# Kernel optimization log

Hardware: AMD Instinct MI355X
Metric: run time of the kernel (lower is better)

The kernel has to match this reference:

```python
import jax, jax.numpy as jnp
import numpy as np

N, K, C, D4, HID, HEAD, DEPTH = 40000, 16, 128, 32, 512, 256, 4
EPS = 1e-5  # BatchNorm eps; eval mode with running_mean=0, running_var=1


def _bn(x, g, b):
    # eval-mode BatchNorm1d with fresh running stats (mean=0, var=1)
    return x * (g / np.sqrt(1.0 + EPS)) + b


def _mlp(x, w1, b1, w2, g, b):
    # Linear -> GELU -> Linear(no bias) -> BN
    return _bn(jax.nn.gelu(x @ w1 + b1) @ w2, g, b)


def _lfp(x, lxyz, knn, proj, coor, scale, g, b):
    # LFP: Linear(no bias) -> la_spse_a4 (neighbor gather + anisotropic spatial
    # positional encoding, one PE channel per 4 feature channels, max-pool over k) -> BN
    xp = x @ proj                                   # (N, C)
    xn = xp[knn]                                    # (N, K, C) irregular gather
    rel3 = (lxyz[knn] - lxyz[:, None])[..., :3]     # (N, K, 3)
    pe = jnp.einsum('nkc,cd->nkd', rel3, coor) * jnp.square(scale)  # (N, K, D4)
    out = jnp.max(xn.reshape(N, K, D4, 4) + pe[..., None], axis=1).reshape(N, C)
    return _bn(out, g, b)


def _knn_spse4(lxyz, feat, knn, m_sp, c, h):
    # knn_spse_4: squared anisotropic spatial distances (3 learned 4-d directions
    # per output channel, 12 params) + per-channel color (3) + height (1) weighted
    # squared diffs, averaged over k neighbors; caller takes sqrt.
    rel4 = lxyz[knn] - lxyz[:, None]                # (N, K, 4)
    relf = feat[knn] - feat[:, None]                # (N, K, 4) = color(3)+height(1)
    dirs = m_sp.reshape(3, 4, C)
    e = jnp.zeros((N, K, C), jnp.float32)
    for j in range(3):  # fixed small loop over 3 learned directions
        e = e + jnp.square(jnp.einsum('nkc,cd->nkd', rel4, dirs[j]))
    e = e + jnp.einsum('nki,id->nkd', jnp.square(relf[..., :3]), jnp.square(c))
    e = e + jnp.square(relf[..., 3:4]) * jnp.square(h)
    return jnp.sqrt(e.mean(axis=1))                 # (N, C)


def setup_inputs():
    key = jax.random.key(0)
    ks = jax.random.split(key, 32)
    rn = lambda i, s, sc=0.02: jax.random.normal(ks[i], s, jnp.float32) * sc
    gm = lambda i, s: 1.0 + jax.random.normal(ks[i], s, jnp.float32) * 0.1
    return {
        'x': rn(0, (N, 4), 1.0),
        'xyz': jax.random.uniform(ks[1], (N, 3), jnp.float32),
        'knn': jax.random.randint(ks[2], (N, K), 0, N, jnp.int32),
        'spse_m': rn(3, (12, C), 0.5),
        'spse_c': rn(4, (3, C), 0.5),
        'spse_h': rn(5, (C,), 0.5),
        'nbr_bn0_g': gm(6, (C,)), 'nbr_bn0_b': rn(7, (C,)),
        'nbr_w1': rn(8, (C, 2 * C)), 'nbr_b1': rn(9, (2 * C,)),
        'nbr_w2': rn(10, (2 * C, C)),
        'nbr_bn_g': gm(11, (C,)), 'nbr_bn_b': rn(12, (C,)),
        'lfp_proj': rn(13, (DEPTH, C, C)),
        'lfp_coor': rn(14, (DEPTH, 3, D4), 0.5),
        'lfp_scale': 0.1 + rn(15, (DEPTH, D4), 0.01),
        'lfp_bng': gm(16, (DEPTH, C)), 'lfp_bnb': rn(17, (DEPTH, C)),
        'mlp_w1': rn(18, (3, C, HID)), 'mlp_b1': rn(19, (3, HID)),
        'mlp_w2': rn(20, (3, HID, C)),
        'mlp_bng': gm(21, (3, C)), 'mlp_bnb': rn(22, (3, C)),
        'post_bn_g': gm(23, (C,)), 'post_bn_b': rn(24, (C,)),
        'post_w': rn(25, (C, HEAD)),
    }


def reference(x, xyz, knn, spse_m, spse_c, spse_h, nbr_bn0_g, nbr_bn0_b,
              nbr_w1, nbr_b1, nbr_w2, nbr_bn_g, nbr_bn_b,
              lfp_proj, lfp_coor, lfp_scale, lfp_bng, lfp_bnb,
              mlp_w1, mlp_b1, mlp_w2, mlp_bng, mlp_bnb,
              post_bn_g, post_bn_b, post_w):
    # Stage.forward, first==last stage, eval mode (no drop_path, no closs).
    lxyz = jnp.pad(xyz, ((0, 0), (0, 1)))  # cor_std = 1.0
    nbr = _knn_spse4(lxyz, x, knn, spse_m, spse_c, spse_h)
    nbr = _bn(nbr, nbr_bn0_g, nbr_bn0_b)
    nbr = jax.nn.gelu(nbr @ nbr_w1 + nbr_b1) @ nbr_w2   # nbr_proj
    h = _bn(nbr, nbr_bn_g, nbr_bn_b)                    # nbr_bn; x = nbr (first stage)
    # Block: residual MLP, then DEPTH LFPs with an MLP after every 2nd LFP
    h = h + _mlp(h, mlp_w1[0], mlp_b1[0], mlp_w2[0], mlp_bng[0], mlp_bnb[0])
    for i in range(DEPTH):
        h = h + _lfp(h, lxyz, knn, lfp_proj[i], lfp_coor[i], lfp_scale[i],
                     lfp_bng[i], lfp_bnb[i])
        if i % 2 == 1:
            j = i // 2 + 1
            h = h + _mlp(h, mlp_w1[j], mlp_b1[j], mlp_w2[j], mlp_bng[j], mlp_bnb[j])
    return _bn(h, post_bn_g, post_bn_b) @ post_w        # postproj -> (N, HEAD)
```

## Files before the change

kernel.cpp:

```cpp
#include <hip/hip_runtime.h>
#include <hip/hip_bf16.h>
#include <math.h>

#define NPTS 40000
#define KNB 16
#define CH 128

typedef unsigned short u16;
typedef __attribute__((ext_vector_type(8))) short bf16x8;
typedef __attribute__((ext_vector_type(4))) float f32x4;

__device__ __forceinline__ float gelu_f(float v) {
  const float u = 0.7978845608028654f * (v + 0.044715f * v * v * v);
  const float t = __builtin_amdgcn_exp2f(-2.8853900817779268f * u);
  return v * __builtin_amdgcn_rcpf(1.0f + t);
}

__device__ __forceinline__ float bnscale(float g) {
  return g * rsqrtf(1.0f + 1e-5f);
}

__device__ __forceinline__ u16 f2bf(float x) {
  union { __hip_bfloat16 b; u16 u; } cv;
  cv.b = __float2bfloat16(x);
  return cv.u;
}

__device__ __forceinline__ float bf2f(u16 u) {
  union { float f; unsigned int i; } cv;
  cv.i = ((unsigned int)u) << 16;
  return cv.f;
}

__device__ __forceinline__ void bf16split(float x, u16& hi, u16& lo) {
  hi = f2bf(x);
  lo = f2bf(x - bf2f(hi));
}

__device__ __forceinline__ void gl2lds(const u16* gp, u16* lp) {
  __builtin_amdgcn_global_load_lds(
      (const __attribute__((address_space(1))) void*)gp,
      (__attribute__((address_space(3))) void*)lp, 16, 0, 0);
}

__global__ __launch_bounds__(128) void spse_kernel(
    const float* __restrict__ x, const float* __restrict__ xyz,
    const int* __restrict__ knn, const float* __restrict__ sm,
    const float* __restrict__ sc, const float* __restrict__ sh,
    const float* __restrict__ g0, const float* __restrict__ b0,
    u16* __restrict__ oh, u16* __restrict__ ol) {
  const int n = blockIdx.x;
  const int c = threadIdx.x;
  __shared__ float sr[KNB][3];
  __shared__ float sf[KNB][4];
  if (c < KNB) {
    const int j = knn[n * KNB + c];
    sr[c][0] = xyz[j * 3 + 0] - xyz[n * 3 + 0];
    sr[c][1] = xyz[j * 3 + 1] - xyz[n * 3 + 1];
    sr[c][2] = xyz[j * 3 + 2] - xyz[n * 3 + 2];
    float f0 = x[j * 4 + 0] - x[n * 4 + 0];
    float f1 = x[j * 4 + 1] - x[n * 4 + 1];
    float f2 = x[j * 4 + 2] - x[n * 4 + 2];
    float f3 = x[j * 4 + 3] - x[n * 4 + 3];
    sf[c][0] = f0 * f0; sf[c][1] = f1 * f1;
    sf[c][2] = f2 * f2; sf[c][3] = f3 * f3;
  }
  __syncthreads();
  const float m0 = sm[c], m1 = sm[CH + c], m2 = sm[2 * CH + c];
  const float m4 = sm[4 * CH + c], m5 = sm[5 * CH + c], m6 = sm[6 * CH + c];
  const float m8 = sm[8 * CH + c], m9 = sm[9 * CH + c], m10 = sm[10 * CH + c];
  float c0 = sc[c];          c0 *= c0;
  float c1 = sc[CH + c];     c1 *= c1;
  float c2 = sc[2 * CH + c]; c2 *= c2;
  float h2 = sh[c];          h2 *= h2;
  float e = 0.0f;
#pragma unroll
  for (int k = 0; k < KNB; k++) {
    const float r0 = sr[k][0], r1 = sr[k][1], r2 = sr[k][2];
    const float d0 = fmaf(r2, m2, fmaf(r1, m1, r0 * m0));
    const float d1 = fmaf(r2, m6, fmaf(r1, m5, r0 * m4));
    const float d2 = fmaf(r2, m10, fmaf(r1, m9, r0 * m8));
    e = fmaf(d0, d0, e);
    e = fmaf(d1, d1, e);
    e = fmaf(d2, d2, e);
    e = fmaf(sf[k][0], c0, e);
    e = fmaf(sf[k][1], c1, e);
    e = fmaf(sf[k][2], c2, e);
    e = fmaf(sf[k][3], h2, e);
  }
  const float v = sqrtf(e * (1.0f / KNB)) * bnscale(g0[c]) + b0[c];
  u16 hi, lo; bf16split(v, hi, lo);
  const size_t idx = (size_t)n * CH + c;
  oh[idx] = hi; ol[idx] = lo;
}

__global__ __launch_bounds__(256) void lfp_kernel(
    const u16* __restrict__ xp, const int* __restrict__ knn,
    const float* __restrict__ xyz, const float* __restrict__ coor,
    const float* __restrict__ scale, const float* __restrict__ g,
    const float* __restrict__ b, u16* __restrict__ hh, u16* __restrict__ hl) {
  const int t = threadIdx.x;
  const int bid = blockIdx.x;
  __shared__ int si[8][KNB];
  __shared__ float sr[8][KNB][3];
  if (t < 128) {
    const int pp = t >> 4, kk = t & 15;
    const int n = bid * 8 + pp;
    const int j = knn[n * KNB + kk];
    si[pp][kk] = j;
    sr[pp][kk][0] = xyz[j * 3 + 0] - xyz[n * 3 + 0];
    sr[pp][kk][1] = xyz[j * 3 + 1] - xyz[n * 3 + 1];
    sr[pp][kk][2] = xyz[j * 3 + 2] - xyz[n * 3 + 2];
  }
  __syncthreads();
  const int p = t >> 5, d = t & 31;
  const int n = bid * 8 + p;
  const float c0 = coor[d], c1 = coor[32 + d], c2 = coor[64 + d];
  float s2 = scale[d]; s2 *= s2;
  float a0 = -3.0e38f, a1 = -3.0e38f, a2 = -3.0e38f, a3 = -3.0e38f;
#pragma unroll
  for (int k = 0; k < KNB; k++) {
    const int j = si[p][k];
    const float pe = fmaf(sr[p][k][2], c2, fmaf(sr[p][k][1], c1, sr[p][k][0] * c0)) * s2;
    const uint2 v = *(const uint2*)(xp + (size_t)j * CH + d * 4);
    a0 = fmaxf(a0, bf2f((u16)(v.x & 0xffff)) + pe);
    a1 = fmaxf(a1, bf2f((u16)(v.x >> 16)) + pe);
    a2 = fmaxf(a2, bf2f((u16)(v.y & 0xffff)) + pe);
    a3 = fmaxf(a3, bf2f((u16)(v.y >> 16)) + pe);
  }
  const size_t off = (size_t)n * CH + d * 4;
  const float4 gg = *(const float4*)(g + d * 4);
  const float4 bb = *(const float4*)(b + d * 4);
  union { u16 a[4]; uint2 v; } oh, olo, ih, il;
  ih.v = *(const uint2*)(hh + off);
  il.v = *(const uint2*)(hl + off);
  float nv[4];
  nv[0] = bf2f(ih.a[0]) + bf2f(il.a[0]) + a0 * bnscale(gg.x) + bb.x;
  nv[1] = bf2f(ih.a[1]) + bf2f(il.a[1]) + a1 * bnscale(gg.y) + bb.y;
  nv[2] = bf2f(ih.a[2]) + bf2f(il.a[2]) + a2 * bnscale(gg.z) + bb.z;
  nv[3] = bf2f(ih.a[3]) + bf2f(il.a[3]) + a3 * bnscale(gg.w) + bb.w;
#pragma unroll
  for (int q = 0; q < 4; q++) {
    u16 hi, lo; bf16split(nv[q], hi, lo);
    oh.a[q] = hi; olo.a[q] = lo;
  }
  *(uint2*)(hh + off) = oh.v;
  *(uint2*)(hl + off) = olo.v;
}

__global__ __launch_bounds__(256) void prep_weights(
    const float* __restrict__ nw1, const float* __restrict__ nw2,
    const float* __restrict__ mw1, const float* __restrict__ mw2,
    const float* __restrict__ lproj, const float* __restrict__ pw,
    const float* __restrict__ pg, u16* __restrict__ th, u16* __restrict__ tl) {
  const int idx = blockIdx.x * 256 + threadIdx.x;
  const float* src;
  int local, Kd, Nd, dst, swz;
  float scale = 1.0f;
  if (idx < 32768)        { src = nw1; local = idx;          Kd = 128; Nd = 256; dst = 0; swz = 0; }
  else if (idx < 65536)   { src = nw2; local = idx - 32768;  Kd = 256; Nd = 128; dst = 32768; swz = 1; }
  else if (idx < 262144)  { int j = (idx - 65536) >> 16;  local = (idx - 65536) & 65535;
                            src = mw1 + j * 65536; Kd = 128; Nd = 512; dst = 65536 + j * 65536; swz = 0; }
  else if (idx < 458752)  { int j = (idx - 262144) >> 16; local = (idx - 262144) & 65535;
                            src = mw2 + j * 65536; Kd = 512; Nd = 128; dst = 262144 + j * 65536; swz = 1; }
  else if (idx < 524288)  { int i = (idx - 458752) >> 14; local = (idx - 458752) & 16383;
                            src = lproj + i * 16384; Kd = 128; Nd = 128; dst = 458752 + i * 16384; swz = 0; }
  else if (idx < 557056)  { local = idx - 524288; src = pw; Kd = 128; Nd = 256; dst = 524288; swz = 0;
                            scale = bnscale(pg[local >> 8]); }
  else return;
  const int k = local / Nd, n = local % Nd;
  const float v = src[local] * scale;
  u16 hi, lo; bf16split(v, hi, lo);
  const int ks = swz ? ((k & ~63) | ((k & 63) ^ ((n & 7) << 3))) : k;
  const int o = dst + n * Kd + ks;
  th[o] = hi; tl[o] = lo;
}

__global__ __launch_bounds__(256) void fold_pb(const float* __restrict__ pw,
                                               const float* __restrict__ pb,
                                               float* __restrict__ fb) {
  const int t = threadIdx.x;
  float a = 0.0f;
  for (int k = 0; k < 128; k++) a = fmaf(pb[k], pw[k * 256 + t], a);
  fb[t] = a;
}

template <int EPI>
__global__ __launch_bounds__(256, 2) void k128_reg(
    const u16* __restrict__ Ahi, const u16* __restrict__ Alo,
    const u16* __restrict__ Wth, const u16* __restrict__ Wtl,
    const float* __restrict__ p0, u16* __restrict__ outu,
    float* __restrict__ outf, int ostride, int ntiles) {
  const int t = threadIdx.x, lane = t & 63, w = t >> 6;
  const int col0 = blockIdx.x * 128;
  const int wm0 = (w >> 1) * 32, wn0 = (w & 1) * 64;
  const int lc = lane & 15, lq = lane >> 4;
  const int lq8 = lq * 8, lq4 = lq * 4;

  bf16x8 wh[4][4], wl[4][4];
  float bv[4];
#pragma unroll
  for (int nf = 0; nf < 4; nf++) {
    const int nr = col0 + wn0 + nf * 16 + lc;
    const u16* wr = Wth + (size_t)nr * 128;
    const u16* wr2 = Wtl + (size_t)nr * 128;
#pragma unroll
    for (int ks = 0; ks < 4; ks++) {
      wh[nf][ks] = *(const bf16x8*)(wr + ks * 32 + lq8);
      wl[nf][ks] = *(const bf16x8*)(wr2 + ks * 32 + lq8);
    }
    bv[nf] = (EPI == 0) ? 0.0f : p0[nr];
  }

  const f32x4 zz = {0.0f, 0.0f, 0.0f, 0.0f};
  for (int tile = blockIdx.y; tile < ntiles; tile += gridDim.y) {
    const int row0 = tile * 64;
    f32x4 acc[2][4];
#pragma unroll
    for (int mf = 0; mf < 2; mf++)
#pragma unroll
      for (int nf = 0; nf < 4; nf++) acc[mf][nf] = zz;
#pragma unroll
    for (int ks = 0; ks < 4; ks++) {
      bf16x8 ah[2], al[2];
#pragma unroll
      for (int mf = 0; mf < 2; mf++) {
        const size_t ao = (size_t)(row0 + wm0 + mf * 16 + lc) * 128 + ks * 32 + lq8;
        ah[mf] = *(const bf16x8*)(Ahi + ao);
        al[mf] = *(const bf16x8*)(Alo + ao);
      }
#pragma unroll
      for (int mf = 0; mf < 2; mf++)
#pragma unroll
        for (int nf = 0; nf < 4; nf++) {
          acc[mf][nf] = __builtin_amdgcn_mfma_f32_16x16x32_bf16(ah[mf], wh[nf][ks], acc[mf][nf], 0, 0, 0);
          acc[mf][nf] = __builtin_amdgcn_mfma_f32_16x16x32_bf16(ah[mf], wl[nf][ks], acc[mf][nf], 0, 0, 0);
          acc[mf][nf] = __builtin_amdgcn_mfma_f32_16x16x32_bf16(al[mf], wh[nf][ks], acc[mf][nf], 0, 0, 0);
        }
    }
#pragma unroll
    for (int mf = 0; mf < 2; mf++)
#pragma unroll
      for (int q = 0; q < 4; q++) {
        const int r = row0 + wm0 + mf * 16 + lq4 + q;
#pragma unroll
        for (int nf = 0; nf < 4; nf++) {
          const int col = col0 + wn0 + nf * 16 + lc;
          const size_t off = (size_t)r * ostride + col;
          const float v = acc[mf][nf][q];
          if (EPI == 0)      outu[off] = f2bf(v);
          else if (EPI == 1) outu[off] = f2bf(gelu_f(v + bv[nf]));
          else               outf[off] = v + bv[nf];
        }
      }
  }
}

template <int K, bool RES>
__global__ __launch_bounds__(512, 4) void gemm_w2(
    const u16* __restrict__ A, const u16* __restrict__ Wth,
    const u16* __restrict__ Wtl, const float* __restrict__ g,
    const float* __restrict__ bb, u16* __restrict__ hh, u16* __restrict__ hl) {
  __shared__ __align__(16) u16 Ws[64 * K];
  const int t = threadIdx.x, lane = t & 63, w = t >> 6;
  const int ch = blockIdx.x;
  const int row0 = blockIdx.y * 256;
  const int msub = w >> 1, cg = w & 1;
  const int lc = lane & 15, lq = lane >> 4;
  const int lq8 = lq * 8, lq4 = lq * 4;

  {
    const u16* src = Wth + (size_t)ch * 64 * K;
#pragma unroll
    for (int i = 0; i < 64 * K / 8; i += 512) {
      const int wc0 = i + w * 64;
      const int c = wc0 + lane;
      gl2lds(src + (size_t)c * 8, Ws + wc0 * 8);
    }
  }
  __syncthreads();

  const int wrow0 = msub * 64;
  const f32x4 zz = {0.0f, 0.0f, 0.0f, 0.0f};
  f32x4 acc[4][2];
#pragma unroll
  for (int mf = 0; mf < 4; mf++)
#pragma unroll
    for (int nf = 0; nf < 2; nf++) acc[mf][nf] = zz;

#pragma unroll 2
  for (int ks = 0; ks < K / 32; ks++) {
    const int e = ks * 32 + lq8;
    bf16x8 af[4];
#pragma unroll
    for (int mf = 0; mf < 4; mf++) {
      int rr = row0 + wrow0 + mf * 16 + lc;
      rr = rr < NPTS ? rr : NPTS - 1;
      af[mf] = *(const bf16x8*)(A + (size_t)rr * K + e);
    }
    bf16x8 whf[2], wlf[2];
#pragma unroll
    for (int nf = 0; nf < 2; nf++) {
      const int nr = cg * 32 + nf * 16 + lc;
      const int eo = (e & ~63) | ((e & 63) ^ ((nr & 7) << 3));
      whf[nf] = *(const bf16x8*)(Ws + nr * K + eo);
      wlf[nf] = *(const bf16x8*)(Wtl + (size_t)(ch * 64 + nr) * K + eo);
    }
#pragma unroll
    for (int mf = 0; mf < 4; mf++)
#pragma unroll
      for (int nf = 0; nf < 2; nf++) {
        acc[mf][nf] = __builtin_amdgcn_mfma_f32_16x16x32_bf16(af[mf], whf[nf], acc[mf][nf], 0, 0, 0);
        acc[mf][nf] = __builtin_amdgcn_mfma_f32_16x16x32_bf16(af[mf], wlf[nf], acc[mf][nf], 0, 0, 0);
      }
  }

  float S0[2], S1[2];
#pragma unroll
  for (int nf = 0; nf < 2; nf++) {
    const int col = ch * 64 + cg * 32 + nf * 16 + lc;
    S0[nf] = bnscale(g[col]);
    S1[nf] = bb[col];
  }
#pragma unroll
  for (int mf = 0; mf < 4; mf++)
#pragma unroll
    for (int q = 0; q < 4; q++) {
      const int r = row0 + wrow0 + mf * 16 + lq4 + q;
      if (r >= NPTS) continue;
#pragma unroll
      for (int nf = 0; nf < 2; nf++) {
        const int col = ch * 64 + cg * 32 + nf * 16 + lc;
        const size_t off = (size_t)r * CH + col;
        float v = acc[mf][nf][q] * S0[nf] + S1[nf];
        if (RES) v += bf2f(hh[off]) + bf2f(hl[off]);
        u16 hi, lo; bf16split(v, hi, lo);
        hh[off] = hi; hl[off] = lo;
      }
    }
}

extern "C" void kernel_launch(void* const* d_in, const int* in_sizes, int n_in,
                              void* d_out, int out_size, void* d_ws, size_t ws_size,
                              hipStream_t stream) {
  const float* x    = (const float*)d_in[0];
  const float* xyz  = (const float*)d_in[1];
  const int*   knn  = (const int*)d_in[2];
  const float* sm   = (const float*)d_in[3];
  const float* scc  = (const float*)d_in[4];
  const float* shh  = (const float*)d_in[5];
  const float* bn0g = (const float*)d_in[6];
  const float* bn0b = (const float*)d_in[7];
  const float* nw1  = (const float*)d_in[8];
  const float* nb1  = (const float*)d_in[9];
  const float* nw2  = (const float*)d_in[10];
  const float* nbng = (const float*)d_in[11];
  const float* nbnb = (const float*)d_in[12];
  const float* lproj  = (const float*)d_in[13];
  const float* lcoor  = (const float*)d_in[14];
  const float* lscale = (const float*)d_in[15];
  const float* lbng   = (const float*)d_in[16];
  const float* lbnb   = (const float*)d_in[17];
  const float* mw1  = (const float*)d_in[18];
  const float* mb1  = (const float*)d_in[19];
  const float* mw2  = (const float*)d_in[20];
  const float* mbng = (const float*)d_in[21];
  const float* mbnb = (const float*)d_in[22];
  const float* pg   = (const float*)d_in[23];
  const float* pb   = (const float*)d_in[24];
  const float* pw   = (const float*)d_in[25];
  float* out = (float*)d_out;

  char* ws = (char*)d_ws;
  u16*   h_hi = (u16*)(ws + 0);
  u16*   h_lo = (u16*)(ws + 10240000);
  u16*   act  = (u16*)(ws + 20480000);
  u16*   xp   = (u16*)(ws + 20480000);
  u16*   Wh   = (u16*)(ws + 61440000);
  u16*   Wl   = (u16*)(ws + 62554112);
  float* fb   = (float*)(ws + 63668224);

  const u16* nw1t   = Wh + 0;
  const u16* nw2t   = Wh + 32768;
  const u16* mw1t   = Wh + 65536;
  const u16* mw2t   = Wh + 262144;
  const u16* lprojt = Wh + 458752;
  const u16* postt  = Wh + 524288;
  const u16* nw1tl   = Wl + 0;
  const u16* nw2tl   = Wl + 32768;
  const u16* mw1tl   = Wl + 65536;
  const u16* mw2tl   = Wl + 262144;
  const u16* lprojtl = Wl + 458752;
  const u16* posttl  = Wl + 524288;

  prep_weights<<<2176, 256, 0, stream>>>(nw1, nw2, mw1, mw2, lproj, pw, pg, Wh, Wl);
  fold_pb<<<1, 256, 0, stream>>>(pw, pb, fb);

  spse_kernel<<<NPTS, 128, 0, stream>>>(x, xyz, knn, sm, scc, shh, bn0g, bn0b, h_hi, h_lo);

  k128_reg<1><<<dim3(2, 256), 256, 0, stream>>>(h_hi, h_lo, nw1t, nw1tl, nb1,
                                                act, nullptr, 256, 625);
  gemm_w2<256, false><<<dim3(2, 157), 512, 0, stream>>>(act, nw2t, nw2tl, nbng, nbnb,
                                                        h_hi, h_lo);
  k128_reg<1><<<dim3(4, 128), 256, 0, stream>>>(h_hi, h_lo, mw1t, mw1tl, mb1,
                                                act, nullptr, 512, 625);
  gemm_w2<512, true><<<dim3(2, 157), 512, 0, stream>>>(act, mw2t, mw2tl, mbng, mbnb,
                                                       h_hi, h_lo);

  for (int i = 0; i < 4; i++) {
    k128_reg<0><<<dim3(1, 512), 256, 0, stream>>>(h_hi, h_lo, lprojt + i * 16384,
                                                  lprojtl + i * 16384, nullptr,
                                                  xp, nullptr, 128, 625);
    lfp_kernel<<<5000, 256, 0, stream>>>(xp, knn, xyz, lcoor + i * 96, lscale + i * 32,
                                         lbng + i * 128, lbnb + i * 128, h_hi, h_lo);
    if (i & 1) {
      const int j = i / 2 + 1;
      k128_reg<1><<<dim3(4, 128), 256, 0, stream>>>(h_hi, h_lo, mw1t + j * 65536,
                                                    mw1tl + j * 65536, mb1 + j * 512,
                                                    act, nullptr, 512, 625);
      gemm_w2<512, true><<<dim3(2, 157), 512, 0, stream>>>(act, mw2t + j * 65536,
                                                           mw2tl + j * 65536,
                                                           mbng + j * 128, mbnb + j * 128,
                                                           h_hi, h_lo);
    }
  }

  k128_reg<2><<<dim3(2, 256), 256, 0, stream>>>(h_hi, h_lo, postt, posttl, fb,
                                                nullptr, out, 256, 625);
}
```

Measured before the change: 529.2 us.

## Restructure W2 GEMM with double-buffered K slabs, widen LFP gather, swap grid axes

The second-layer GEMM now gives each block a 64-row tile across all 128 output columns. It streams 64-wide K slabs of the high weight half into double-buffered LDS while prefetching the next A fragments, instead of staging the whole 64xK weight slice once per column chunk. The LFP kernel handles 16 points per block with 16-byte gathers of 8 channels per thread, which uses every thread in the index staging phase and widens the memory accesses. k128_reg swaps grid axes so consecutive blocks walk row tiles and the launches are remapped to match. The gains sought are better load/compute overlap, wider memory transactions and better cache locality, at the cost of more barriers and higher register use per thread.

```diff
diff --git a/kernel.cpp b/kernel.cpp
--- a/kernel.cpp
+++ b/kernel.cpp
@@ -101,11 +101,11 @@
     const float* __restrict__ b, u16* __restrict__ hh, u16* __restrict__ hl) {
   const int t = threadIdx.x;
   const int bid = blockIdx.x;
-  __shared__ int si[8][KNB];
-  __shared__ float sr[8][KNB][3];
-  if (t < 128) {
+  __shared__ int si[16][KNB];
+  __shared__ float sr[16][KNB][3];
+  {
     const int pp = t >> 4, kk = t & 15;
-    const int n = bid * 8 + pp;
+    const int n = bid * 16 + pp;
     const int j = knn[n * KNB + kk];
     si[pp][kk] = j;
     sr[pp][kk][0] = xyz[j * 3 + 0] - xyz[n * 3 + 0];
@@ -113,39 +113,40 @@
     sr[pp][kk][2] = xyz[j * 3 + 2] - xyz[n * 3 + 2];
   }
   __syncthreads();
-  const int p = t >> 5, d = t & 31;
-  const int n = bid * 8 + p;
-  const float c0 = coor[d], c1 = coor[32 + d], c2 = coor[64 + d];
-  float s2 = scale[d]; s2 *= s2;
-  float a0 = -3.0e38f, a1 = -3.0e38f, a2 = -3.0e38f, a3 = -3.0e38f;
+  const int p = t >> 4, d8 = t & 15;
+  const int n = bid * 16 + p;
+  const float c0a = coor[d8 * 2],     c1a = coor[32 + d8 * 2],     c2a = coor[64 + d8 * 2];
+  const float c0b = coor[d8 * 2 + 1], c1b = coor[32 + d8 * 2 + 1], c2b = coor[64 + d8 * 2 + 1];
+  float s2a = scale[d8 * 2];     s2a *= s2a;
+  float s2b = scale[d8 * 2 + 1]; s2b *= s2b;
+  float a[8];
+#pragma unroll
+  for (int e = 0; e < 8; e++) a[e] = -3.0e38f;
 #pragma unroll
   for (int k = 0; k < KNB; k++) {
     const int j = si[p][k];
-    const float pe = fmaf(sr[p][k][2], c2, fmaf(sr[p][k][1], c1, sr[p][k][0] * c0)) * s2;
-    const uint2 v = *(const uint2*)(xp + (size_t)j * CH + d * 4);
-    a0 = fmaxf(a0, bf2f((u16)(v.x & 0xffff)) + pe);
-    a1 = fmaxf(a1, bf2f((u16)(v.x >> 16)) + pe);
-    a2 = fmaxf(a2, bf2f((u16)(v.y & 0xffff)) + pe);
-    a3 = fmaxf(a3, bf2f((u16)(v.y >> 16)) + pe);
-  }
-  const size_t off = (size_t)n * CH + d * 4;
-  const float4 gg = *(const float4*)(g + d * 4);
-  const float4 bb = *(const float4*)(b + d * 4);
-  union { u16 a[4]; uint2 v; } oh, olo, ih, il;
-  ih.v = *(const uint2*)(hh + off);
-  il.v = *(const uint2*)(hl + off);
-  float nv[4];
-  nv[0] = bf2f(ih.a[0]) + bf2f(il.a[0]) + a0 * bnscale(gg.x) + bb.x;
-  nv[1] = bf2f(ih.a[1]) + bf2f(il.a[1]) + a1 * bnscale(gg.y) + bb.y;
-  nv[2] = bf2f(ih.a[2]) + bf2f(il.a[2]) + a2 * bnscale(gg.z) + bb.z;
-  nv[3] = bf2f(ih.a[3]) + bf2f(il.a[3]) + a3 * bnscale(gg.w) + bb.w;
-#pragma unroll
-  for (int q = 0; q < 4; q++) {
-    u16 hi, lo; bf16split(nv[q], hi, lo);
-    oh.a[q] = hi; olo.a[q] = lo;
-  }
-  *(uint2*)(hh + off) = oh.v;
-  *(uint2*)(hl + off) = olo.v;
+    const float r0 = sr[p][k][0], r1 = sr[p][k][1], r2 = sr[p][k][2];
+    const float pea = fmaf(r2, c2a, fmaf(r1, c1a, r0 * c0a)) * s2a;
+    const float peb = fmaf(r2, c2b, fmaf(r1, c1b, r0 * c0b)) * s2b;
+    const bf16x8 v = *(const bf16x8*)(xp + (size_t)j * CH + d8 * 8);
+#pragma unroll
+    for (int e = 0; e < 4; e++) a[e] = fmaxf(a[e], bf2f((u16)v[e]) + pea);
+#pragma unroll
+    for (int e = 4; e < 8; e++) a[e] = fmaxf(a[e], bf2f((u16)v[e]) + peb);
+  }
+  const size_t off = (size_t)n * CH + d8 * 8;
+  union { u16 a[8]; uint4 v; } ih, il, oh, ol;
+  ih.v = *(const uint4*)(hh + off);
+  il.v = *(const uint4*)(hl + off);
+#pragma unroll
+  for (int e = 0; e < 8; e++) {
+    const int c = d8 * 8 + e;
+    const float nv = bf2f(ih.a[e]) + bf2f(il.a[e]) + a[e] * bnscale(g[c]) + b[c];
+    u16 hi, lo; bf16split(nv, hi, lo);
+    oh.a[e] = hi; ol.a[e] = lo;
+  }
+  *(uint4*)(hh + off) = oh.v;
+  *(uint4*)(hl + off) = ol.v;
 }
 
 __global__ __launch_bounds__(256) void prep_weights(
@@ -192,7 +193,7 @@
     const float* __restrict__ p0, u16* __restrict__ outu,
     float* __restrict__ outf, int ostride, int ntiles) {
   const int t = threadIdx.x, lane = t & 63, w = t >> 6;
-  const int col0 = blockIdx.x * 128;
+  const int col0 = blockIdx.y * 128;
   const int wm0 = (w >> 1) * 32, wn0 = (w & 1) * 64;
   const int lc = lane & 15, lq = lane >> 4;
   const int lq8 = lq * 8, lq4 = lq * 4;
@@ -213,7 +214,7 @@
   }
 
   const f32x4 zz = {0.0f, 0.0f, 0.0f, 0.0f};
-  for (int tile = blockIdx.y; tile < ntiles; tile += gridDim.y) {
+  for (int tile = blockIdx.x; tile < ntiles; tile += gridDim.x) {
     const int row0 = tile * 64;
     f32x4 acc[2][4];
 #pragma unroll
@@ -257,80 +258,94 @@
 }
 
 template <int K, bool RES>
-__global__ __launch_bounds__(512, 4) void gemm_w2(
+__global__ __launch_bounds__(256, 3) void gemm_w2(
     const u16* __restrict__ A, const u16* __restrict__ Wth,
     const u16* __restrict__ Wtl, const float* __restrict__ g,
     const float* __restrict__ bb, u16* __restrict__ hh, u16* __restrict__ hl) {
-  __shared__ __align__(16) u16 Ws[64 * K];
+  __shared__ __align__(16) u16 Ws[2][128 * 64];
   const int t = threadIdx.x, lane = t & 63, w = t >> 6;
-  const int ch = blockIdx.x;
-  const int row0 = blockIdx.y * 256;
-  const int msub = w >> 1, cg = w & 1;
+  const int row0 = blockIdx.x * 64;
+  const int wm0 = (w >> 1) * 32, wn0 = (w & 1) * 64;
   const int lc = lane & 15, lq = lane >> 4;
   const int lq8 = lq * 8, lq4 = lq * 4;
 
-  {
-    const u16* src = Wth + (size_t)ch * 64 * K;
-#pragma unroll
-    for (int i = 0; i < 64 * K / 8; i += 512) {
+  const f32x4 zz = {0.0f, 0.0f, 0.0f, 0.0f};
+  f32x4 acc[2][4];
+#pragma unroll
+  for (int mf = 0; mf < 2; mf++)
+#pragma unroll
+    for (int nf = 0; nf < 4; nf++) acc[mf][nf] = zz;
+
+  auto stage_slab = [&](u16* lds, int kb) {
+#pragma unroll
+    for (int i = 0; i < 1024; i += 256) {
       const int wc0 = i + w * 64;
       const int c = wc0 + lane;
-      gl2lds(src + (size_t)c * 8, Ws + wc0 * 8);
-    }
-  }
+      gl2lds(Wth + (size_t)(c >> 3) * K + kb + (c & 7) * 8, lds + wc0 * 8);
+    }
+  };
+  auto load_af = [&](bf16x8 (&dst)[2][2], int kb) {
+#pragma unroll
+    for (int mf = 0; mf < 2; mf++)
+#pragma unroll
+      for (int ks = 0; ks < 2; ks++)
+        dst[mf][ks] = *(const bf16x8*)(A + (size_t)(row0 + wm0 + mf * 16 + lc) * K +
+                                       kb + ks * 32 + lq8);
+  };
+
+  bf16x8 afc[2][2], afn[2][2];
+  stage_slab(Ws[0], 0);
+  load_af(afc, 0);
   __syncthreads();
 
-  const int wrow0 = msub * 64;
-  const f32x4 zz = {0.0f, 0.0f, 0.0f, 0.0f};
-  f32x4 acc[4][2];
-#pragma unroll
-  for (int mf = 0; mf < 4; mf++)
-#pragma unroll
-    for (int nf = 0; nf < 2; nf++) acc[mf][nf] = zz;
-
+  constexpr int NT = K / 64;
 #pragma unroll 2
-  for (int ks = 0; ks < K / 32; ks++) {
-    const int e = ks * 32 + lq8;
-    bf16x8 af[4];
-#pragma unroll
-    for (int mf = 0; mf < 4; mf++) {
-      int rr = row0 + wrow0 + mf * 16 + lc;
-      rr = rr < NPTS ? rr : NPTS - 1;
-      af[mf] = *(const bf16x8*)(A + (size_t)rr * K + e);
-    }
-    bf16x8 whf[2], wlf[2];
-#pragma unroll
-    for (int nf = 0; nf < 2; nf++) {
-      const int nr = cg * 32 + nf * 16 + lc;
-      const int eo = (e & ~63) | ((e & 63) ^ ((nr & 7) << 3));
-      whf[nf] = *(const bf16x8*)(Ws + nr * K + eo);
-      wlf[nf] = *(const bf16x8*)(Wtl + (size_t)(ch * 64 + nr) * K + eo);
-    }
-#pragma unroll
-    for (int mf = 0; mf < 4; mf++)
-#pragma unroll
-      for (int nf = 0; nf < 2; nf++) {
-        acc[mf][nf] = __builtin_amdgcn_mfma_f32_16x16x32_bf16(af[mf], whf[nf], acc[mf][nf], 0, 0, 0);
-        acc[mf][nf] = __builtin_amdgcn_mfma_f32_16x16x32_bf16(af[mf], wlf[nf], acc[mf][nf], 0, 0, 0);
+  for (int tt = 0; tt < NT; tt++) {
+    const int cur = tt & 1;
+    if (tt + 1 < NT) {
+      stage_slab(Ws[cur ^ 1], (tt + 1) * 64);
+      load_af(afn, (tt + 1) * 64);
+    }
+#pragma unroll
+    for (int ks = 0; ks < 2; ks++) {
+      bf16x8 whf[4], wlf[4];
+#pragma unroll
+      for (int nf = 0; nf < 4; nf++) {
+        const int nr = wn0 + nf * 16 + lc;
+        const int j = (ks * 32 + lq8) ^ ((nr & 7) << 3);
+        whf[nf] = *(const bf16x8*)(Ws[cur] + nr * 64 + j);
+        wlf[nf] = *(const bf16x8*)(Wtl + (size_t)nr * K + tt * 64 + j);
       }
-  }
-
-  float S0[2], S1[2];
-#pragma unroll
-  for (int nf = 0; nf < 2; nf++) {
-    const int col = ch * 64 + cg * 32 + nf * 16 + lc;
+#pragma unroll
+      for (int mf = 0; mf < 2; mf++)
+#pragma unroll
+        for (int nf = 0; nf < 4; nf++) {
+          acc[mf][nf] = __builtin_amdgcn_mfma_f32_16x16x32_bf16(afc[mf][ks], whf[nf], acc[mf][nf], 0, 0, 0);
+          acc[mf][nf] = __builtin_amdgcn_mfma_f32_16x16x32_bf16(afc[mf][ks], wlf[nf], acc[mf][nf], 0, 0, 0);
+        }
+    }
+    __syncthreads();
+#pragma unroll
+    for (int mf = 0; mf < 2; mf++)
+#pragma unroll
+      for (int ks = 0; ks < 2; ks++) afc[mf][ks] = afn[mf][ks];
+  }
+
+  float S0[4], S1[4];
+#pragma unroll
+  for (int nf = 0; nf < 4; nf++) {
+    const int col = wn0 + nf * 16 + lc;
     S0[nf] = bnscale(g[col]);
     S1[nf] = bb[col];
   }
 #pragma unroll
-  for (int mf = 0; mf < 4; mf++)
+  for (int mf = 0; mf < 2; mf++)
 #pragma unroll
     for (int q = 0; q < 4; q++) {
-      const int r = row0 + wrow0 + mf * 16 + lq4 + q;
-      if (r >= NPTS) continue;
-#pragma unroll
-      for (int nf = 0; nf < 2; nf++) {
-        const int col = ch * 64 + cg * 32 + nf * 16 + lc;
+      const int r = row0 + wm0 + mf * 16 + lq4 + q;
+#pragma unroll
+      for (int nf = 0; nf < 4; nf++) {
+        const int col = wn0 + nf * 16 + lc;
         const size_t off = (size_t)r * CH + col;
         float v = acc[mf][nf][q] * S0[nf] + S1[nf];
         if (RES) v += bf2f(hh[off]) + bf2f(hl[off]);
@@ -398,33 +413,31 @@
 
   spse_kernel<<<NPTS, 128, 0, stream>>>(x, xyz, knn, sm, scc, shh, bn0g, bn0b, h_hi, h_lo);
 
-  k128_reg<1><<<dim3(2, 256), 256, 0, stream>>>(h_hi, h_lo, nw1t, nw1tl, nb1,
+  k128_reg<1><<<dim3(256, 2), 256, 0, stream>>>(h_hi, h_lo, nw1t, nw1tl, nb1,
                                                 act, nullptr, 256, 625);
-  gemm_w2<256, false><<<dim3(2, 157), 512, 0, stream>>>(act, nw2t, nw2tl, nbng, nbnb,
-                                                        h_hi, h_lo);
-  k128_reg<1><<<dim3(4, 128), 256, 0, stream>>>(h_hi, h_lo, mw1t, mw1tl, mb1,
+  gemm_w2<256, false><<<625, 256, 0, stream>>>(act, nw2t, nw2tl, nbng, nbnb, h_hi, h_lo);
+
+  k128_reg<1><<<dim3(128, 4), 256, 0, stream>>>(h_hi, h_lo, mw1t, mw1tl, mb1,
                                                 act, nullptr, 512, 625);
-  gemm_w2<512, true><<<dim3(2, 157), 512, 0, stream>>>(act, mw2t, mw2tl, mbng, mbnb,
-                                                       h_hi, h_lo);
+  gemm_w2<512, true><<<625, 256, 0, stream>>>(act, mw2t, mw2tl, mbng, mbnb, h_hi, h_lo);
 
   for (int i = 0; i < 4; i++) {
-    k128_reg<0><<<dim3(1, 512), 256, 0, stream>>>(h_hi, h_lo, lprojt + i * 16384,
+    k128_reg<0><<<dim3(625, 1), 256, 0, stream>>>(h_hi, h_lo, lprojt + i * 16384,
                                                   lprojtl + i * 16384, nullptr,
                                                   xp, nullptr, 128, 625);
-    lfp_kernel<<<5000, 256, 0, stream>>>(xp, knn, xyz, lcoor + i * 96, lscale + i * 32,
+    lfp_kernel<<<2500, 256, 0, stream>>>(xp, knn, xyz, lcoor + i * 96, lscale + i * 32,
                                          lbng + i * 128, lbnb + i * 128, h_hi, h_lo);
     if (i & 1) {
       const int j = i / 2 + 1;
-      k128_reg<1><<<dim3(4, 128), 256, 0, stream>>>(h_hi, h_lo, mw1t + j * 65536,
+      k128_reg<1><<<dim3(128, 4), 256, 0, stream>>>(h_hi, h_lo, mw1t + j * 65536,
                                                     mw1tl + j * 65536, mb1 + j * 512,
                                                     act, nullptr, 512, 625);
-      gemm_w2<512, true><<<dim3(2, 157), 512, 0, stream>>>(act, mw2t + j * 65536,
-                                                           mw2tl + j * 65536,
-                                                           mbng + j * 128, mbnb + j * 128,
-                                                           h_hi, h_lo);
-    }
-  }
-
-  k128_reg<2><<<dim3(2, 256), 256, 0, stream>>>(h_hi, h_lo, postt, posttl, fb,
+      gemm_w2<512, true><<<625, 256, 0, stream>>>(act, mw2t + j * 65536, mw2tl + j * 65536,
+                                                  mbng + j * 128, mbnb + j * 128,
+                                                  h_hi, h_lo);
+    }
+  }
+
+  k128_reg<2><<<dim3(256, 2), 256, 0, stream>>>(h_hi, h_lo, postt, posttl, fb,
                                                 nullptr, out, 256, 625);
 }
```

Measured after the change: 497.2 us. 1.06x faster.
